# Kernel optimization log

Hardware: AMD Instinct MI355X
Metric: run time of the kernel (lower is better)

The kernel has to match this reference:

```python
import jax
import jax.numpy as jnp
import numpy as np

N = 256   # hardcoded in the torch module via expand(256, 256)
D = 256
K = 16
M_MARGIN = 0.6
T_THRESH = 0.0025
EPS = 1e-12


def setup_inputs() -> dict:
    key = jax.random.key(0)
    k1, k2 = jax.random.split(key)
    yi = jax.random.normal(k1, (N, D), dtype=jnp.float32)
    yi_t = jax.random.normal(k2, (N, D), dtype=jnp.float32)
    return {"yi": yi, "yi_t": yi_t}


def _l2_normalize(x):
    return x / jnp.sqrt(jnp.sum(x * x, axis=-1, keepdims=True) + EPS)


def reference(yi, yi_t):
    yi_n = _l2_normalize(yi)      # [N, D]
    yit_n = _l2_normalize(yi_t)   # [N, D]

    # pairwise half-distances: [N, N]
    diff = yi_n[:, None, :] - yi_n[None, :, :]           # [N, N, D]
    dis_yii = 0.5 * jnp.sqrt(jnp.sum(diff * diff, axis=-1) + EPS)

    # K+1 smallest distances per row (self is smallest)
    neg_vals, topk_idx = jax.lax.top_k(-dis_yii, K + 1)  # [N, K+1]
    nbr_idx = topk_idx[:, 1:]                            # [N, K] exclude self

    yj = yi_n[nbr_idx]                                   # [N, K, D]
    dis_yij = 0.5 * jnp.sqrt(jnp.sum((yi_n[:, None, :] - yj) ** 2, axis=-1) + EPS)
    dis_yi_tj = 0.5 * jnp.sqrt(jnp.sum((yit_n[:, None, :] - yj) ** 2, axis=-1) + EPS)

    e1 = jnp.sum((dis_yij - dis_yi_tj) ** 2 - T_THRESH)

    # margin term: dist(yi, yi_t) + m - (second smallest pairwise dist)
    dis_yi_yi_t = 0.5 * jnp.sqrt(jnp.sum((yi_n - yit_n) ** 2, axis=-1) + EPS)  # [N]
    second_nn = -neg_vals[:, 1]                          # [N]
    out = dis_yi_yi_t + M_MARGIN - second_nn
    e2 = jnp.sum(jnp.maximum(out, 0.0))

    return e1 + e2
```

## Files before the change

### kernel.cpp

```cpp
#include <hip/hip_runtime.h>
#include <math.h>

#define NN 256
#define DD 256
#define KK 16
#define M_MARGIN 0.6f
#define T_THRESH 0.0025f
#define EPS 1e-12f

__global__ void __launch_bounds__(512) blcd_fused_kernel(
    const float* __restrict__ yi, const float* __restrict__ yit,
    float* __restrict__ out)
{
    __shared__ float s_yi[DD];
    __shared__ float s_yit[DD];
    __shared__ float sdis[NN];
    __shared__ float red[24];

    const int i = blockIdx.x;
    const int t = threadIdx.x;
    const int j = t >> 1;
    const int h = t & 1;

    float a = 0.0f, b = 0.0f;
    if (t < DD) {
        a = yi [i * DD + t];
        b = yit[i * DD + t];
        s_yi[t]  = a;
        s_yit[t] = b;
    }
    float r0 = a * a, r1 = b * b, r2 = a * b;
    #pragma unroll
    for (int off = 32; off > 0; off >>= 1) {
        r0 += __shfl_down(r0, off, 64);
        r1 += __shfl_down(r1, off, 64);
        r2 += __shfl_down(r2, off, 64);
    }
    const int w = t >> 6;
    if ((t & 63) == 0) { red[w] = r0; red[8 + w] = r1; red[16 + w] = r2; }
    __syncthreads();

    const float nn_i  = ((red[0]  + red[1])  + (red[2]  + red[3]))
                      + ((red[4]  + red[5])  + (red[6]  + red[7]));
    const float nn_it = ((red[8]  + red[9])  + (red[10] + red[11]))
                      + ((red[12] + red[13]) + (red[14] + red[15]));
    const float cross = ((red[16] + red[17]) + (red[18] + red[19]))
                      + ((red[20] + red[21]) + (red[22] + red[23]));
    const float inv_ni  = 1.0f / sqrtf(nn_i  + EPS);
    const float inv_nit = 1.0f / sqrtf(nn_it + EPS);

    const float4* __restrict__ rj  = (const float4*)(yi + j * DD);
    const float4* __restrict__ si  = (const float4*)s_yi;
    const float4* __restrict__ sit = (const float4*)s_yit;
    float4 q4  = make_float4(0.f, 0.f, 0.f, 0.f);
    float4 qt4 = make_float4(0.f, 0.f, 0.f, 0.f);
    float4 nn4 = make_float4(0.f, 0.f, 0.f, 0.f);
    #pragma unroll 8
    for (int k = 0; k < DD / 8; ++k) {
        const int d4 = 2 * k + h;
        float4 y = rj[d4];
        float4 u = si[d4];
        float4 v = sit[d4];
        q4.x  += y.x * u.x; q4.y  += y.y * u.y; q4.z  += y.z * u.z; q4.w  += y.w * u.w;
        qt4.x += y.x * v.x; qt4.y += y.y * v.y; qt4.z += y.z * v.z; qt4.w += y.w * v.w;
        nn4.x += y.x * y.x; nn4.y += y.y * y.y; nn4.z += y.z * y.z; nn4.w += y.w * y.w;
    }
    float q  = (q4.x  + q4.y ) + (q4.z  + q4.w );
    float qt = (qt4.x + qt4.y) + (qt4.z + qt4.w);
    float nn = (nn4.x + nn4.y) + (nn4.z + nn4.w);
    q  += __shfl_xor(q,  1, 64);
    qt += __shfl_xor(qt, 1, 64);
    nn += __shfl_xor(nn, 1, 64);

    const float inv_nt = 1.0f / sqrtf(nn + EPS);
    const float c    = q  * inv_nt * inv_ni;
    const float ct   = qt * inv_nt * inv_nit;
    const float myv  = 0.5f * sqrtf(fmaxf(2.0f - 2.0f * c , 0.0f) + EPS);
    const float myvt = 0.5f * sqrtf(fmaxf(2.0f - 2.0f * ct, 0.0f) + EPS);
    if (h == 0) sdis[j] = myv;
    __syncthreads();

    int rank = 0;
    const float4* sd4 = (const float4*)sdis;
    #pragma unroll 8
    for (int k = h * (NN / 8); k < (h + 1) * (NN / 8); ++k) {
        float4 v = sd4[k];
        const int jj = k * 4;
        rank += (v.x < myv || (v.x == myv && (jj + 0) < j)) ? 1 : 0;
        rank += (v.y < myv || (v.y == myv && (jj + 1) < j)) ? 1 : 0;
        rank += (v.z < myv || (v.z == myv && (jj + 2) < j)) ? 1 : 0;
        rank += (v.w < myv || (v.w == myv && (jj + 3) < j)) ? 1 : 0;
    }
    rank += __shfl_xor(rank, 1, 64);

    float contrib = 0.0f;
    if (h == 0) {
        if (rank >= 1 && rank <= KK) {
            const float dd = myv - myvt;
            contrib = dd * dd - T_THRESH;
        }
        if (rank == 1) {
            const float cc = cross * inv_ni * inv_nit;
            const float d_iit = 0.5f * sqrtf(fmaxf(2.0f - 2.0f * cc, 0.0f) + EPS);
            contrib += fmaxf(d_iit + M_MARGIN - myv, 0.0f);
        }
    }

    #pragma unroll
    for (int off = 32; off > 0; off >>= 1) contrib += __shfl_down(contrib, off, 64);
    __syncthreads();
    if ((t & 63) == 0) red[w] = contrib;
    __syncthreads();
    if (t == 0)
        atomicAdd(out, ((red[0] + red[1]) + (red[2] + red[3]))
                     + ((red[4] + red[5]) + (red[6] + red[7])));
}

extern "C" void kernel_launch(void* const* d_in, const int* in_sizes, int n_in,
                              void* d_out, int out_size, void* d_ws, size_t ws_size,
                              hipStream_t stream) {
    (void)in_sizes; (void)n_in; (void)out_size; (void)d_ws; (void)ws_size;

    const float* yi  = (const float*)d_in[0];
    const float* yit = (const float*)d_in[1];
    float* out = (float*)d_out;

    hipMemsetAsync(out, 0, sizeof(float), stream);
    blcd_fused_kernel<<<NN, 512, 0, stream>>>(yi, yit, out);
}
```

Before: 69.67 us.

## Use 1024 threads per row, prefetch neighbor rows, replace atomic with reduce kernel

Each block now uses 4 threads per candidate row instead of 2, and the whole 256-float row slice is loaded into registers before the first barrier so global-load latency overlaps the norm reduction. The memset plus atomicAdd is replaced by per-block partial sums written to workspace and a second single-block reduce kernel, which makes the final sum deterministic. The cost is an extra kernel launch and 64 float registers per thread at 1024-thread blocks, which may limit occupancy.

Result: faster. 64.30 us (-7.7%).

```diff
diff --git a/kernel.cpp b/kernel.cpp
--- a/kernel.cpp
+++ b/kernel.cpp
@@ -8,27 +8,34 @@
 #define T_THRESH 0.0025f
 #define EPS 1e-12f
 
-__global__ void __launch_bounds__(512) blcd_fused_kernel(
+__global__ void __launch_bounds__(1024) blcd_row_kernel(
     const float* __restrict__ yi, const float* __restrict__ yit,
-    float* __restrict__ out)
+    float* __restrict__ partial)
 {
     __shared__ float s_yi[DD];
     __shared__ float s_yit[DD];
     __shared__ float sdis[NN];
-    __shared__ float red[24];
+    __shared__ float red[48];
 
     const int i = blockIdx.x;
     const int t = threadIdx.x;
-    const int j = t >> 1;
-    const int h = t & 1;
+    const int j = t >> 2;
+    const int s = t & 3;
+    const int w = t >> 6;
 
     float a = 0.0f, b = 0.0f;
     if (t < DD) {
         a = yi [i * DD + t];
         b = yit[i * DD + t];
-        s_yi[t]  = a;
-        s_yit[t] = b;
     }
+
+    const float4* __restrict__ rj = (const float4*)(yi + j * DD);
+    float4 p[16];
+    #pragma unroll
+    for (int k = 0; k < 16; ++k) p[k] = rj[4 * k + s];
+
+    if (t < DD) { s_yi[t] = a; s_yit[t] = b; }
+
     float r0 = a * a, r1 = b * b, r2 = a * b;
     #pragma unroll
     for (int off = 32; off > 0; off >>= 1) {
@@ -36,29 +43,24 @@
         r1 += __shfl_down(r1, off, 64);
         r2 += __shfl_down(r2, off, 64);
     }
-    const int w = t >> 6;
-    if ((t & 63) == 0) { red[w] = r0; red[8 + w] = r1; red[16 + w] = r2; }
+    if ((t & 63) == 0) { red[w] = r0; red[16 + w] = r1; red[32 + w] = r2; }
     __syncthreads();
 
-    const float nn_i  = ((red[0]  + red[1])  + (red[2]  + red[3]))
-                      + ((red[4]  + red[5])  + (red[6]  + red[7]));
-    const float nn_it = ((red[8]  + red[9])  + (red[10] + red[11]))
-                      + ((red[12] + red[13]) + (red[14] + red[15]));
-    const float cross = ((red[16] + red[17]) + (red[18] + red[19]))
-                      + ((red[20] + red[21]) + (red[22] + red[23]));
+    const float nn_i  = (red[0]  + red[1])  + (red[2]  + red[3]);
+    const float nn_it = (red[16] + red[17]) + (red[18] + red[19]);
+    const float cross = (red[32] + red[33]) + (red[34] + red[35]);
     const float inv_ni  = 1.0f / sqrtf(nn_i  + EPS);
     const float inv_nit = 1.0f / sqrtf(nn_it + EPS);
 
-    const float4* __restrict__ rj  = (const float4*)(yi + j * DD);
     const float4* __restrict__ si  = (const float4*)s_yi;
     const float4* __restrict__ sit = (const float4*)s_yit;
     float4 q4  = make_float4(0.f, 0.f, 0.f, 0.f);
     float4 qt4 = make_float4(0.f, 0.f, 0.f, 0.f);
     float4 nn4 = make_float4(0.f, 0.f, 0.f, 0.f);
-    #pragma unroll 8
-    for (int k = 0; k < DD / 8; ++k) {
-        const int d4 = 2 * k + h;
-        float4 y = rj[d4];
+    #pragma unroll
+    for (int k = 0; k < 16; ++k) {
+        const int d4 = 4 * k + s;
+        float4 y = p[k];
         float4 u = si[d4];
         float4 v = sit[d4];
         q4.x  += y.x * u.x; q4.y  += y.y * u.y; q4.z  += y.z * u.z; q4.w  += y.w * u.w;
@@ -68,22 +70,23 @@
     float q  = (q4.x  + q4.y ) + (q4.z  + q4.w );
     float qt = (qt4.x + qt4.y) + (qt4.z + qt4.w);
     float nn = (nn4.x + nn4.y) + (nn4.z + nn4.w);
-    q  += __shfl_xor(q,  1, 64);
-    qt += __shfl_xor(qt, 1, 64);
-    nn += __shfl_xor(nn, 1, 64);
+    q  += __shfl_xor(q,  1, 64);  q  += __shfl_xor(q,  2, 64);
+    qt += __shfl_xor(qt, 1, 64);  qt += __shfl_xor(qt, 2, 64);
+    nn += __shfl_xor(nn, 1, 64);  nn += __shfl_xor(nn, 2, 64);
 
     const float inv_nt = 1.0f / sqrtf(nn + EPS);
     const float c    = q  * inv_nt * inv_ni;
     const float ct   = qt * inv_nt * inv_nit;
     const float myv  = 0.5f * sqrtf(fmaxf(2.0f - 2.0f * c , 0.0f) + EPS);
     const float myvt = 0.5f * sqrtf(fmaxf(2.0f - 2.0f * ct, 0.0f) + EPS);
-    if (h == 0) sdis[j] = myv;
+    if (s == 0) sdis[j] = myv;
     __syncthreads();
 
     int rank = 0;
     const float4* sd4 = (const float4*)sdis;
-    #pragma unroll 8
-    for (int k = h * (NN / 8); k < (h + 1) * (NN / 8); ++k) {
+    #pragma unroll
+    for (int m = 0; m < 16; ++m) {
+        const int k = 4 * m + s;
         float4 v = sd4[k];
         const int jj = k * 4;
         rank += (v.x < myv || (v.x == myv && (jj + 0) < j)) ? 1 : 0;
@@ -92,9 +95,10 @@
         rank += (v.w < myv || (v.w == myv && (jj + 3) < j)) ? 1 : 0;
     }
     rank += __shfl_xor(rank, 1, 64);
+    rank += __shfl_xor(rank, 2, 64);
 
     float contrib = 0.0f;
-    if (h == 0) {
+    if (s == 0) {
         if (rank >= 1 && rank <= KK) {
             const float dd = myv - myvt;
             contrib = dd * dd - T_THRESH;
@@ -108,23 +112,40 @@
 
     #pragma unroll
     for (int off = 32; off > 0; off >>= 1) contrib += __shfl_down(contrib, off, 64);
-    __syncthreads();
     if ((t & 63) == 0) red[w] = contrib;
     __syncthreads();
-    if (t == 0)
-        atomicAdd(out, ((red[0] + red[1]) + (red[2] + red[3]))
-                     + ((red[4] + red[5]) + (red[6] + red[7])));
+    if (t == 0) {
+        float tot = ((red[0]  + red[1])  + (red[2]  + red[3]))
+                  + ((red[4]  + red[5])  + (red[6]  + red[7]))
+                  + ((red[8]  + red[9])  + (red[10] + red[11]))
+                  + ((red[12] + red[13]) + (red[14] + red[15]));
+        partial[i] = tot;
+    }
+}
+
+__global__ void __launch_bounds__(NN) blcd_reduce_kernel(
+    const float* __restrict__ partial, float* __restrict__ out)
+{
+    __shared__ float red[4];
+    const int t = threadIdx.x;
+    float v = partial[t];
+    #pragma unroll
+    for (int off = 32; off > 0; off >>= 1) v += __shfl_down(v, off, 64);
+    if ((t & 63) == 0) red[t >> 6] = v;
+    __syncthreads();
+    if (t == 0) out[0] = (red[0] + red[1]) + (red[2] + red[3]);
 }
 
 extern "C" void kernel_launch(void* const* d_in, const int* in_sizes, int n_in,
                               void* d_out, int out_size, void* d_ws, size_t ws_size,
                               hipStream_t stream) {
-    (void)in_sizes; (void)n_in; (void)out_size; (void)d_ws; (void)ws_size;
+    (void)in_sizes; (void)n_in; (void)out_size; (void)ws_size;
 
     const float* yi  = (const float*)d_in[0];
     const float* yit = (const float*)d_in[1];
     float* out = (float*)d_out;
+    float* ws  = (float*)d_ws;
 
-    hipMemsetAsync(out, 0, sizeof(float), stream);
-    blcd_fused_kernel<<<NN, 512, 0, stream>>>(yi, yit, out);
+    blcd_row_kernel<<<NN, 1024, 0, stream>>>(yi, yit, ws);
+    blcd_reduce_kernel<<<1, NN, 0, stream>>>(ws, out);
 }
```
